# Kernel optimization log

Hardware: AMD Instinct MI355X
Metric: run time of the kernel (lower is better)

Reference implementation:

```python
import jax, jax.numpy as jnp
import numpy as np

NUM_CLASSES = 21
IOU_THRESH = 0.5
NEG_POS_RATIO = 3
VAR0, VAR1 = 0.1, 0.2


def point_form(priors):
    # (cx,cy,w,h) -> (xmin,ymin,xmax,ymax)
    return jnp.concatenate([priors[:, :2] - priors[:, 2:] / 2,
                            priors[:, :2] + priors[:, 2:] / 2], axis=-1)


def jaccard(box_a, box_b):
    # box_a: [n,4] point form, box_b: [N,4] point form -> [n,N]
    max_xy = jnp.minimum(box_a[:, None, 2:], box_b[None, :, 2:])
    min_xy = jnp.maximum(box_a[:, None, :2], box_b[None, :, :2])
    inter = jnp.prod(jnp.clip(max_xy - min_xy, 0.0, None), axis=-1)
    area_a = jnp.prod(box_a[:, 2:] - box_a[:, :2], axis=-1)[:, None]
    area_b = jnp.prod(box_b[:, 2:] - box_b[:, :2], axis=-1)[None, :]
    return inter / (area_a + area_b - inter)


def encode(matched, priors):
    # matched: [N,4] point form, priors: [N,4] center form
    g_cxcy = ((matched[:, :2] + matched[:, 2:]) / 2 - priors[:, :2]) / (VAR0 * priors[:, 2:])
    g_wh = jnp.log((matched[:, 2:] - matched[:, :2]) / priors[:, 2:]) / VAR1
    return jnp.concatenate([g_cxcy, g_wh], axis=-1)


def match_one(truths, labels, priors):
    # truths: [n_obj,4], labels: [n_obj], priors: [N,4] center form
    ov = jaccard(truths, point_form(priors))          # [n_obj, N]
    best_prior_idx = jnp.argmax(ov, axis=1)           # [n_obj]
    best_truth_overlap = jnp.max(ov, axis=0)          # [N]
    best_truth_idx = jnp.argmax(ov, axis=0)           # [N]
    best_truth_overlap = best_truth_overlap.at[best_prior_idx].set(2.0)
    def body(j, bti):
        return bti.at[best_prior_idx[j]].set(j)
    best_truth_idx = jax.lax.fori_loop(0, truths.shape[0], body, best_truth_idx)
    matched = truths[best_truth_idx]                  # [N,4]
    conf = labels[best_truth_idx].astype(jnp.int32) + 1
    conf = jnp.where(best_truth_overlap < IOU_THRESH, 0, conf)
    return encode(matched, priors), conf


def smooth_l1(x):
    ax = jnp.abs(x)
    return jnp.where(ax < 1.0, 0.5 * x * x, ax - 0.5)


def setup_inputs() -> dict:
    key = jax.random.key(0)
    k1, k2, k3, k4, k5, k6, k7 = jax.random.split(key, 7)
    B, N, n_obj = 128, 8732, 16
    loc_data = jax.random.normal(k1, (B, N, 4), jnp.float32)
    conf_data = jax.random.normal(k2, (B, N, NUM_CLASSES), jnp.float32)
    # valid ground-truth boxes in [0,1], point form, plus class label in [0,20)
    mins = jax.random.uniform(k3, (B, n_obj, 2)) * 0.6
    sizes = jax.random.uniform(k4, (B, n_obj, 2)) * 0.35 + 0.05
    labels = jax.random.randint(k5, (B, n_obj), 0, NUM_CLASSES - 1).astype(jnp.float32)
    targets = jnp.concatenate([mins, mins + sizes, labels[..., None]], axis=-1)
    # priors in center form with positive w,h
    centers = jax.random.uniform(k6, (N, 2))
    wh = jax.random.uniform(k7, (N, 2)) * 0.5 + 0.05
    priors = jnp.concatenate([centers, wh], axis=-1).astype(jnp.float32)
    return {"loc_data": loc_data, "conf_data": conf_data, "targets": targets, "priors": priors}


def _forward(loc_data, conf_data, targets, priors):
    B, N = loc_data.shape[0], loc_data.shape[1]
    truths, labels = targets[:, :, :4], targets[:, :, 4]
    target_loc, target_conf = jax.vmap(match_one, in_axes=(0, 0, None))(truths, labels, priors)
    pos = target_conf > 0                             # [B,N]
    # localization: smooth-L1 summed over positive priors
    loss_l = jnp.sum(smooth_l1(loc_data - target_loc) * pos[..., None].astype(loc_data.dtype))
    # per-prior CE surrogate: logsumexp - logit[target]
    lse = jax.nn.logsumexp(conf_data, axis=-1)        # [B,N]
    gathered = jnp.take_along_axis(conf_data, target_conf[..., None], axis=-1)[..., 0]
    loss_c_all = lse - gathered                       # [B,N]
    # hard negative mining via double argsort ranking (positives excluded)
    lc = jnp.where(pos, 0.0, loss_c_all)
    loss_idx = jnp.argsort(-lc, axis=1)
    idx_rank = jnp.argsort(loss_idx, axis=1)
    num_pos = jnp.sum(pos.astype(jnp.int32), axis=1, keepdims=True)   # [B,1]
    num_neg = jnp.minimum(NEG_POS_RATIO * num_pos, N - 1)
    neg = idx_rank < num_neg
    sel = pos | neg
    loss_c = jnp.sum(jnp.where(sel, loss_c_all, 0.0))
    n_total = jnp.sum(num_pos).astype(loc_data.dtype)
    return loss_l / n_total, loss_c / n_total


def reference(loc_data, conf_data, targets, priors):
    return _forward(loc_data, conf_data, targets, priors)
```

## Files before the change

kernel.cpp:

```cpp
#include <hip/hip_runtime.h>
#include <cstdint>
#include <cstddef>

#define HB1 4096
#define HB2 2048
#define CMAX 21
#define IOU_T 0.5f

__device__ __forceinline__ float sl1(float x) {
    float ax = fabsf(x);
    return ax < 1.0f ? 0.5f * x * x : ax - 0.5f;
}

__global__ __launch_bounds__(256) void kA_best_prior(
    const float* __restrict__ targets, const float* __restrict__ priors,
    float* __restrict__ bpi_val, int* __restrict__ bpi_idx,
    int* __restrict__ num_pos_g, float* __restrict__ accB_g,
    float* __restrict__ acc_g, unsigned* __restrict__ done_g,
    int N, int NOBJ, int SLICES, int CHUNK, int B)
{
    const int s = blockIdx.x, b = blockIdx.y, t = threadIdx.x;
    __shared__ float tb[16 * 4];
    __shared__ float ta[16];
    __shared__ float wv[4 * 16];
    __shared__ int   wi[4 * 16];

    if (s == 0 && b == 0) {
        for (int q = t; q < B; q += 256) num_pos_g[q] = 0;
        for (int q = t; q < 2 * B; q += 256) accB_g[q] = 0.f;
        if (t < 4) acc_g[t] = 0.f;
        if (t == 0) *done_g = 0u;
    }

    if (t < 16) {
        if (t < NOBJ) {
            const float* tr = targets + ((size_t)b * NOBJ + t) * 5;
            float x0 = tr[0], y0 = tr[1], x1 = tr[2], y1 = tr[3];
            tb[t * 4 + 0] = x0; tb[t * 4 + 1] = y0;
            tb[t * 4 + 2] = x1; tb[t * 4 + 3] = y1;
            ta[t] = (x1 - x0) * (y1 - y0);
        } else {
            tb[t * 4 + 0] = 0.f; tb[t * 4 + 1] = 0.f;
            tb[t * 4 + 2] = 0.f; tb[t * 4 + 3] = 0.f;
            ta[t] = 0.f;
        }
    }
    __syncthreads();

    float bv[16]; int bi[16];
#pragma unroll
    for (int j = 0; j < 16; j++) { bv[j] = -1.0f; bi[j] = 0x7fffffff; }

    const int start = s * CHUNK;
    const int end = min(start + CHUNK, N);
    for (int i = start + t; i < end; i += 256) {
        float4 p = ((const float4*)priors)[i];
        float bx0 = p.x - p.z * 0.5f, by0 = p.y - p.w * 0.5f;
        float bx1 = p.x + p.z * 0.5f, by1 = p.y + p.w * 0.5f;
        float ab = (bx1 - bx0) * (by1 - by0);
#pragma unroll
        for (int j = 0; j < 16; j++) {
            float iw = fminf(tb[j * 4 + 2], bx1) - fmaxf(tb[j * 4 + 0], bx0);
            float ih = fminf(tb[j * 4 + 3], by1) - fmaxf(tb[j * 4 + 1], by0);
            iw = fmaxf(iw, 0.f); ih = fmaxf(ih, 0.f);
            float inter = iw * ih;
            float iou = inter / (ta[j] + ab - inter);
            if (iou > bv[j] || (iou == bv[j] && i < bi[j])) { bv[j] = iou; bi[j] = i; }
        }
    }

#pragma unroll
    for (int off = 32; off >= 1; off >>= 1) {
#pragma unroll
        for (int j = 0; j < 16; j++) {
            float v2 = __shfl_down(bv[j], off, 64);
            int   i2 = __shfl_down(bi[j], off, 64);
            if (v2 > bv[j] || (v2 == bv[j] && i2 < bi[j])) { bv[j] = v2; bi[j] = i2; }
        }
    }
    const int wid = t >> 6, lane = t & 63;
    if (lane == 0) {
#pragma unroll
        for (int j = 0; j < 16; j++) { wv[wid * 16 + j] = bv[j]; wi[wid * 16 + j] = bi[j]; }
    }
    __syncthreads();
    if (t < 16) {
        float v = wv[t]; int idx = wi[t];
#pragma unroll
        for (int w = 1; w < 4; w++) {
            float v2 = wv[w * 16 + t]; int i2 = wi[w * 16 + t];
            if (v2 > v || (v2 == v && i2 < idx)) { v = v2; idx = i2; }
        }
        if (t < NOBJ) {
            int o = (b * SLICES + s) * 16 + t;
            bpi_val[o] = v;
            bpi_idx[o] = idx;
        }
    }
}

#define IOU_STEP(j) { \
    float4 tj = tb4[j]; \
    float taj = (tj.z - tj.x) * (tj.w - tj.y); \
    float iw = fminf(tj.z, bx1) - fmaxf(tj.x, bx0); \
    float ih = fminf(tj.w, by1) - fmaxf(tj.y, by0); \
    iw = fmaxf(iw, 0.f); ih = fmaxf(ih, 0.f); \
    float inter = iw * ih; \
    float iou = inter * __builtin_amdgcn_rcpf(taj + ab - inter); \
    if (iou > bto) { bto = iou; bti = (j); } }

__global__ __launch_bounds__(256, 3) void kB_main(
    const float* __restrict__ loc, const float* __restrict__ conf,
    const float* __restrict__ targets, const float* __restrict__ priors,
    const float* __restrict__ bpi_val, const int* __restrict__ bpi_idx,
    float* __restrict__ lc_out, int* __restrict__ num_pos, float* __restrict__ accB,
    int N, int NOBJ, int SLICES, int TPB, int BPB)
{
    const int g = blockIdx.x;
    const int b = g / BPB;
    const int j0 = g % BPB;
    const int t = threadIdx.x;
    const int wid = t >> 6, lane = t & 63;

    __shared__ __align__(16) float buf[2][256 * CMAX];
    __shared__ __align__(16) float tb[16 * 4];
    __shared__ float tl[16];
    __shared__ __align__(16) int bpi_s[16];
    __shared__ float wred[4 * 3];

    if (t < 16) {
        if (t < NOBJ) {
            const float* tr = targets + ((size_t)b * NOBJ + t) * 5;
            tb[t * 4 + 0] = tr[0]; tb[t * 4 + 1] = tr[1];
            tb[t * 4 + 2] = tr[2]; tb[t * 4 + 3] = tr[3];
            tl[t] = tr[4];
            float bv = -1.f; int bi = 0x7fffffff;
            for (int s2 = 0; s2 < SLICES; s2++) {
                int o = (b * SLICES + s2) * 16 + t;
                float v = bpi_val[o]; int idx = bpi_idx[o];
                if (v > bv || (v == bv && idx < bi)) { bv = v; bi = idx; }
            }
            bpi_s[t] = bi;
        } else {
            tb[t * 4 + 0] = 0.f; tb[t * 4 + 1] = 0.f; tb[t * 4 + 2] = 0.f; tb[t * 4 + 3] = 0.f;
            tl[t] = 0.f; bpi_s[t] = -1;
        }
    }

    const float* confB = conf + (size_t)b * N * CMAX;
    const float* locB  = loc + (size_t)b * N * 4;

    float4 r0, r1, r2, r3, r4, r5, pld, ppr;

    auto stage = [&](int xx) {
        int i0s = xx * 256;
        int rows_s = min(256, N - i0s);
        int nf4s = (rows_s * CMAX) >> 2;
        const float4* s4 = (const float4*)(confB + (size_t)i0s * CMAX);
        if (t + 0    < nf4s) r0 = s4[t + 0];
        if (t + 256  < nf4s) r1 = s4[t + 256];
        if (t + 512  < nf4s) r2 = s4[t + 512];
        if (t + 768  < nf4s) r3 = s4[t + 768];
        if (t + 1024 < nf4s) r4 = s4[t + 1024];
        if (t + 1280 < nf4s) r5 = s4[t + 1280];
        if (t < rows_s) {
            ppr = ((const float4*)priors)[i0s + t];
            pld = ((const float4*)locB)[i0s + t];
        }
    };

    float ll = 0.f, plc = 0.f, np = 0.f;
    int x = j0, p = 0;
    if (x < TPB) stage(x);

    while (x < TPB) {
        const int i0 = x * 256;
        const int rows = min(256, N - i0);
        const int nf4 = (rows * CMAX) >> 2;

        float4 myp = ppr, myl = pld;

        float4* bp4f = (float4*)buf[p];
        if (t + 0    < nf4) bp4f[t + 0]    = r0;
        if (t + 256  < nf4) bp4f[t + 256]  = r1;
        if (t + 512  < nf4) bp4f[t + 512]  = r2;
        if (t + 768  < nf4) bp4f[t + 768]  = r3;
        if (t + 1024 < nf4) bp4f[t + 1024] = r4;
        if (t + 1280 < nf4) bp4f[t + 1280] = r5;
        __syncthreads();

        int xn = x + BPB;
        if (xn < TPB) stage(xn);

        if (t < rows) {
            const int i = i0 + t;
            float4 pp = myp;
            float bx0 = pp.x - pp.z * 0.5f, by0 = pp.y - pp.w * 0.5f;
            float bx1 = pp.x + pp.z * 0.5f, by1 = pp.y + pp.w * 0.5f;
            float ab = (bx1 - bx0) * (by1 - by0);
            float bto = -1.f; int bti = 0;
            const float4* tb4 = (const float4*)tb;
            if (NOBJ == 16) {
#pragma unroll
                for (int j = 0; j < 16; j++) IOU_STEP(j);
            } else {
                for (int j = 0; j < NOBJ; j++) IOU_STEP(j);
            }
            const int4* bp4 = (const int4*)bpi_s;
#pragma unroll
            for (int jj = 0; jj < 4; jj++) {
                int4 q = bp4[jj];
                if (q.x == i) { bto = 2.0f; bti = jj * 4 + 0; }
                if (q.y == i) { bto = 2.0f; bti = jj * 4 + 1; }
                if (q.z == i) { bto = 2.0f; bti = jj * 4 + 2; }
                if (q.w == i) { bto = 2.0f; bti = jj * 4 + 3; }
            }
            bool pos = !(bto < IOU_T);
            if (pos) {
                float4 tj = tb4[bti];
                float rz = __builtin_amdgcn_rcpf(pp.z);
                float rw = __builtin_amdgcn_rcpf(pp.w);
                float gcx = ((tj.x + tj.z) * 0.5f - pp.x) * (10.0f * rz);
                float gcy = ((tj.y + tj.w) * 0.5f - pp.y) * (10.0f * rw);
                float gw = __logf((tj.z - tj.x) * rz) * 5.0f;
                float gh = __logf((tj.w - tj.y) * rw) * 5.0f;
                ll += sl1(myl.x - gcx) + sl1(myl.y - gcy) + sl1(myl.z - gw) + sl1(myl.w - gh);
                np += 1.f;
            }
            int cf = pos ? ((int)tl[bti] + 1) : 0;
            const float* cr = buf[p] + t * CMAX;
            float m = cr[0];
#pragma unroll
            for (int c = 1; c < CMAX; c++) m = fmaxf(m, cr[c]);
            float ssum = 0.f;
#pragma unroll
            for (int c = 0; c < CMAX; c++) ssum += __expf(cr[c] - m);
            float lse = m + __logf(ssum);
            float lossc = lse - cr[cf];
            if (pos) plc += lossc;
            float lcv = pos ? 0.f : lossc;
            lcv = fmaxf(lcv, 0.f);
            lc_out[(size_t)b * N + i] = lcv;
        }
        p ^= 1;
        x = xn;
    }

#pragma unroll
    for (int off = 32; off >= 1; off >>= 1) {
        ll  += __shfl_down(ll, off, 64);
        plc += __shfl_down(plc, off, 64);
        np  += __shfl_down(np, off, 64);
    }
    if (lane == 0) { wred[wid * 3 + 0] = ll; wred[wid * 3 + 1] = plc; wred[wid * 3 + 2] = np; }
    __syncthreads();
    if (t == 0) {
        float a0 = 0.f, a1 = 0.f, a2 = 0.f;
#pragma unroll
        for (int w = 0; w < 4; w++) { a0 += wred[w * 3 + 0]; a1 += wred[w * 3 + 1]; a2 += wred[w * 3 + 2]; }
        atomicAdd(&accB[b * 2 + 0], a0);
        atomicAdd(&accB[b * 2 + 1], a1);
        atomicAdd(&num_pos[b], (int)a2);
    }
}

__device__ __forceinline__ void suffix_scan(int* cnt, float* sm, int n, int t, int nt) {
    for (int d = 1; d < n; d <<= 1) {
        int tc[8]; float ts[8];
        int r = 0;
        for (int q = t; q < n; q += nt, r++) {
            int src = q + d;
            tc[r] = (src < n) ? cnt[src] : 0;
            ts[r] = (src < n) ? sm[src] : 0.f;
        }
        __syncthreads();
        r = 0;
        for (int q = t; q < n; q += nt, r++) { cnt[q] += tc[r]; sm[q] += ts[r]; }
        __syncthreads();
    }
}

__global__ __launch_bounds__(512) void kC_topk(
    const float* __restrict__ lc, const int* __restrict__ num_pos,
    const float* __restrict__ accB,
    float* __restrict__ acc, unsigned* __restrict__ done_ctr,
    float* __restrict__ out, int N, int B)
{
    const int b = blockIdx.x, t = threadIdx.x;
    const int NT = 512;
    __shared__ int cnt[HB1];
    __shared__ float sm[HB1];
    __shared__ int s_strad, s_krem;
    __shared__ float s_above;
    __shared__ int s_last;
    __shared__ float wsum[8], wsA[8], wsB[8];

    const int k = min(3 * num_pos[b], N - 1);
    const float* lcb = lc + (size_t)b * N;
    float total = 0.f;

    if (k > 0) {
        for (int q = t; q < HB1; q += NT) { cnt[q] = 0; sm[q] = 0.f; }
        __syncthreads();
        const int n4 = N >> 2;
        const float4* lcb4 = (const float4*)lcb;
        for (int i = t; i < n4; i += NT) {
            float4 v = lcb4[i];
            { unsigned u = __float_as_uint(v.x) >> 19; atomicAdd(&cnt[u], 1); atomicAdd(&sm[u], v.x); }
            { unsigned u = __float_as_uint(v.y) >> 19; atomicAdd(&cnt[u], 1); atomicAdd(&sm[u], v.y); }
            { unsigned u = __float_as_uint(v.z) >> 19; atomicAdd(&cnt[u], 1); atomicAdd(&sm[u], v.z); }
            { unsigned u = __float_as_uint(v.w) >> 19; atomicAdd(&cnt[u], 1); atomicAdd(&sm[u], v.w); }
        }
        for (int i = (n4 << 2) + t; i < N; i += NT) {
            float v = lcb[i];
            unsigned u = __float_as_uint(v) >> 19;
            atomicAdd(&cnt[u], 1); atomicAdd(&sm[u], v);
        }
        __syncthreads();
        suffix_scan(cnt, sm, HB1, t, NT);
        for (int q = t; q < HB1; q += NT) {
            int incl = cnt[q];
            int excl = (q < HB1 - 1) ? cnt[q + 1] : 0;
            if (excl < k && k <= incl) {
                s_strad = q; s_krem = k - excl;
                s_above = (q < HB1 - 1) ? sm[q + 1] : 0.f;
            }
        }
        __syncthreads();
        int s1 = s_strad, k2 = s_krem;
        total += s_above;
        __syncthreads();

        for (int q = t; q < HB2; q += NT) { cnt[q] = 0; sm[q] = 0.f; }
        __syncthreads();
        for (int i = t; i < N; i += NT) {
            float v = lcb[i];
            unsigned u = __float_as_uint(v);
            if ((int)(u >> 19) == s1) {
                int q = (int)((u >> 8) & 0x7FF);
                atomicAdd(&cnt[q], 1); atomicAdd(&sm[q], v);
            }
        }
        __syncthreads();
        suffix_scan(cnt, sm, HB2, t, NT);
        for (int q = t; q < HB2; q += NT) {
            int incl = cnt[q];
            int excl = (q < HB2 - 1) ? cnt[q + 1] : 0;
            if (excl < k2 && k2 <= incl) {
                s_strad = q; s_krem = k2 - excl;
                s_above = (q < HB2 - 1) ? sm[q + 1] : 0.f;
            }
        }
        __syncthreads();
        int s2 = s_strad, krem = s_krem;
        total += s_above;
        float tval = __uint_as_float((((unsigned)s1) << 19) | (((unsigned)s2) << 8));
        total += (float)krem * tval;
    }

    if (t == 0) {
        if (k > 0) atomicAdd(&acc[1], total);
        __threadfence();
        unsigned old = atomicAdd(done_ctr, 1u);
        s_last = (old == (unsigned)gridDim.x - 1u) ? 1 : 0;
    }
    __syncthreads();
    if (s_last) {
        __threadfence();
        float vn = 0.f, va = 0.f, vb = 0.f;
        for (int q = t; q < B; q += NT) {
            vn += (float)num_pos[q];
            va += accB[q * 2 + 0];
            vb += accB[q * 2 + 1];
        }
#pragma unroll
        for (int off = 32; off >= 1; off >>= 1) {
            vn += __shfl_down(vn, off, 64);
            va += __shfl_down(va, off, 64);
            vb += __shfl_down(vb, off, 64);
        }
        if ((t & 63) == 0) { wsum[t >> 6] = vn; wsA[t >> 6] = va; wsB[t >> 6] = vb; }
        __syncthreads();
        if (t == 0) {
            float n = 0.f, a = 0.f, bsum = 0.f;
#pragma unroll
            for (int w = 0; w < 8; w++) { n += wsum[w]; a += wsA[w]; bsum += wsB[w]; }
            float l2 = atomicAdd(&acc[1], 0.0f);
            out[0] = a / n;
            out[1] = (bsum + l2) / n;
        }
    }
}

extern "C" void kernel_launch(void* const* d_in, const int* in_sizes, int n_in,
                              void* d_out, int out_size, void* d_ws, size_t ws_size,
                              hipStream_t stream)
{
    const float* loc     = (const float*)d_in[0];
    const float* conf    = (const float*)d_in[1];
    const float* targets = (const float*)d_in[2];
    const float* priors  = (const float*)d_in[3];
    float* out = (float*)d_out;

    const int N = in_sizes[3] / 4;
    const int BN = in_sizes[0] / 4;
    const int B = BN / N;
    const int NOBJ = in_sizes[2] / (B * 5);
    const int SLICES = 8;
    const int CHUNK = (N + SLICES - 1) / SLICES;
    const int TPB = (N + 255) / 256;
    const int BPB = 6;

    char* w = (char*)d_ws;
    float*    lc_ws   = (float*)w;                         size_t off = (size_t)BN * 4;
    float*    bpi_val = (float*)(w + off);                 off += (size_t)B * SLICES * 16 * 4;
    int*      bpi_idx = (int*)(w + off);                   off += (size_t)B * SLICES * 16 * 4;
    int*      num_pos = (int*)(w + off);                   off += (size_t)B * 4;
    float*    accB    = (float*)(w + off);                 off += (size_t)B * 2 * 4;
    float*    acc     = (float*)(w + off);                 off += 16;
    unsigned* done    = (unsigned*)(w + off);              off += 16;

    dim3 gA(SLICES, B);
    kA_best_prior<<<gA, 256, 0, stream>>>(targets, priors, bpi_val, bpi_idx,
                                          num_pos, accB, acc, done, N, NOBJ, SLICES, CHUNK, B);

    kB_main<<<B * BPB, 256, 0, stream>>>(loc, conf, targets, priors, bpi_val, bpi_idx,
                                         lc_ws, num_pos, accB, N, NOBJ, SLICES, TPB, BPB);

    kC_topk<<<B, 512, 0, stream>>>(lc_ws, num_pos, accB, acc, done, out, N, B);
}
```

Measured before the change: 261.2 us.

## Replace shared-memory Hillis-Steele suffix scan with wave-shuffle scan in top-k kernel

The histogram-based top-k kernel replaces its log-step shared-memory suffix scan over 4096/2048 bins with a per-thread vector load, a 64-lane shuffle suffix scan and a cross-wave combine. The block size doubles to 1024 threads so each thread owns exactly 4 or 2 bins. This removes the many barrier-separated passes over shared memory. The trade-off is a larger block, which may lower occupancy and raise contention on the shared-memory histogram atomics.

```diff
diff --git a/kernel.cpp b/kernel.cpp
--- a/kernel.cpp
+++ b/kernel.cpp
@@ -264,43 +264,40 @@
     }
 }
 
-__device__ __forceinline__ void suffix_scan(int* cnt, float* sm, int n, int t, int nt) {
-    for (int d = 1; d < n; d <<= 1) {
-        int tc[8]; float ts[8];
-        int r = 0;
-        for (int q = t; q < n; q += nt, r++) {
-            int src = q + d;
-            tc[r] = (src < n) ? cnt[src] : 0;
-            ts[r] = (src < n) ? sm[src] : 0.f;
-        }
-        __syncthreads();
-        r = 0;
-        for (int q = t; q < n; q += nt, r++) { cnt[q] += tc[r]; sm[q] += ts[r]; }
-        __syncthreads();
-    }
-}
-
-__global__ __launch_bounds__(512) void kC_topk(
+__device__ __forceinline__ void wave_sufscan(int& c, float& s, int lane) {
+#pragma unroll
+    for (int off = 1; off < 64; off <<= 1) {
+        int c2 = __shfl_down(c, off, 64);
+        float s2 = __shfl_down(s, off, 64);
+        if (lane + off < 64) { c += c2; s += s2; }
+    }
+}
+
+__global__ __launch_bounds__(1024) void kC_topk(
     const float* __restrict__ lc, const int* __restrict__ num_pos,
     const float* __restrict__ accB,
     float* __restrict__ acc, unsigned* __restrict__ done_ctr,
     float* __restrict__ out, int N, int B)
 {
     const int b = blockIdx.x, t = threadIdx.x;
-    const int NT = 512;
-    __shared__ int cnt[HB1];
-    __shared__ float sm[HB1];
+    const int NT = 1024;
+    const int wid = t >> 6, lane = t & 63;
+    __shared__ __align__(16) int   cnt[HB1];
+    __shared__ __align__(16) float sm[HB1];
+    __shared__ int   wc[16];
+    __shared__ float ws[16];
     __shared__ int s_strad, s_krem;
     __shared__ float s_above;
     __shared__ int s_last;
-    __shared__ float wsum[8], wsA[8], wsB[8];
+    __shared__ float wsum[16], wsA[16], wsB[16];
 
     const int k = min(3 * num_pos[b], N - 1);
     const float* lcb = lc + (size_t)b * N;
     float total = 0.f;
 
     if (k > 0) {
-        for (int q = t; q < HB1; q += NT) { cnt[q] = 0; sm[q] = 0.f; }
+        ((int4*)cnt)[t] = make_int4(0, 0, 0, 0);
+        ((float4*)sm)[t] = make_float4(0.f, 0.f, 0.f, 0.f);
         __syncthreads();
         const int n4 = N >> 2;
         const float4* lcb4 = (const float4*)lcb;
@@ -317,21 +314,33 @@
             atomicAdd(&cnt[u], 1); atomicAdd(&sm[u], v);
         }
         __syncthreads();
-        suffix_scan(cnt, sm, HB1, t, NT);
-        for (int q = t; q < HB1; q += NT) {
-            int incl = cnt[q];
-            int excl = (q < HB1 - 1) ? cnt[q + 1] : 0;
-            if (excl < k && k <= incl) {
-                s_strad = q; s_krem = k - excl;
-                s_above = (q < HB1 - 1) ? sm[q + 1] : 0.f;
-            }
-        }
-        __syncthreads();
-        int s1 = s_strad, k2 = s_krem;
+        {
+            int4  cv = ((const int4*)cnt)[t];
+            float4 sv = ((const float4*)sm)[t];
+            int   ci = cv.x + cv.y + cv.z + cv.w;
+            float si = sv.x + sv.y + sv.z + sv.w;
+            wave_sufscan(ci, si, lane);
+            if (lane == 0) { wc[wid] = ci; ws[wid] = si; }
+            __syncthreads();
+            int cab = 0; float sab = 0.f;
+            for (int w = wid + 1; w < 16; w++) { cab += wc[w]; sab += ws[w]; }
+            int   i0c = ci + cab;          float f0 = si + sab;
+            int   i1c = i0c - cv.x;        float f1 = f0 - sv.x;
+            int   i2c = i1c - cv.y;        float f2 = f1 - sv.y;
+            int   i3c = i2c - cv.z;        float f3 = f2 - sv.z;
+            int   i4c = i3c - cv.w;
+            if (i1c < k && k <= i0c) { s_strad = 4 * t + 0; s_krem = k - i1c; s_above = f1; }
+            if (i2c < k && k <= i1c) { s_strad = 4 * t + 1; s_krem = k - i2c; s_above = f2; }
+            if (i3c < k && k <= i2c) { s_strad = 4 * t + 2; s_krem = k - i3c; s_above = f3; }
+            if (i4c < k && k <= i3c) { s_strad = 4 * t + 3; s_krem = k - i4c; s_above = f3 - sv.w; }
+        }
+        __syncthreads();
+        const int s1 = s_strad, k2 = s_krem;
         total += s_above;
-        __syncthreads();
-
-        for (int q = t; q < HB2; q += NT) { cnt[q] = 0; sm[q] = 0.f; }
+
+        __syncthreads();
+        ((int2*)cnt)[t] = make_int2(0, 0);
+        ((float2*)sm)[t] = make_float2(0.f, 0.f);
         __syncthreads();
         for (int i = t; i < N; i += NT) {
             float v = lcb[i];
@@ -342,17 +351,24 @@
             }
         }
         __syncthreads();
-        suffix_scan(cnt, sm, HB2, t, NT);
-        for (int q = t; q < HB2; q += NT) {
-            int incl = cnt[q];
-            int excl = (q < HB2 - 1) ? cnt[q + 1] : 0;
-            if (excl < k2 && k2 <= incl) {
-                s_strad = q; s_krem = k2 - excl;
-                s_above = (q < HB2 - 1) ? sm[q + 1] : 0.f;
-            }
-        }
-        __syncthreads();
-        int s2 = s_strad, krem = s_krem;
+        {
+            int2  cv = ((const int2*)cnt)[t];
+            float2 sv = ((const float2*)sm)[t];
+            int   ci = cv.x + cv.y;
+            float si = sv.x + sv.y;
+            wave_sufscan(ci, si, lane);
+            if (lane == 0) { wc[wid] = ci; ws[wid] = si; }
+            __syncthreads();
+            int cab = 0; float sab = 0.f;
+            for (int w = wid + 1; w < 16; w++) { cab += wc[w]; sab += ws[w]; }
+            int   i0c = ci + cab;       float f0 = si + sab;
+            int   i1c = i0c - cv.x;     float f1 = f0 - sv.x;
+            int   i2c = i1c - cv.y;
+            if (i1c < k2 && k2 <= i0c) { s_strad = 2 * t + 0; s_krem = k2 - i1c; s_above = f1; }
+            if (i2c < k2 && k2 <= i1c) { s_strad = 2 * t + 1; s_krem = k2 - i2c; s_above = f1 - sv.y; }
+        }
+        __syncthreads();
+        const int s2 = s_strad, krem = s_krem;
         total += s_above;
         float tval = __uint_as_float((((unsigned)s1) << 19) | (((unsigned)s2) << 8));
         total += (float)krem * tval;
@@ -379,12 +395,12 @@
             va += __shfl_down(va, off, 64);
             vb += __shfl_down(vb, off, 64);
         }
-        if ((t & 63) == 0) { wsum[t >> 6] = vn; wsA[t >> 6] = va; wsB[t >> 6] = vb; }
+        if (lane == 0) { wsum[wid] = vn; wsA[wid] = va; wsB[wid] = vb; }
         __syncthreads();
         if (t == 0) {
             float n = 0.f, a = 0.f, bsum = 0.f;
 #pragma unroll
-            for (int w = 0; w < 8; w++) { n += wsum[w]; a += wsA[w]; bsum += wsB[w]; }
+            for (int w = 0; w < 16; w++) { n += wsum[w]; a += wsA[w]; bsum += wsB[w]; }
             float l2 = atomicAdd(&acc[1], 0.0f);
             out[0] = a / n;
             out[1] = (bsum + l2) / n;
@@ -427,5 +443,5 @@
     kB_main<<<B * BPB, 256, 0, stream>>>(loc, conf, targets, priors, bpi_val, bpi_idx,
                                          lc_ws, num_pos, accB, N, NOBJ, SLICES, TPB, BPB);
 
-    kC_topk<<<B, 512, 0, stream>>>(lc_ws, num_pos, accB, acc, done, out, N, B);
-}
+    kC_topk<<<B, 1024, 0, stream>>>(lc_ws, num_pos, accB, acc, done, out, N, B);
+}
```

Result: faster. 225.7 us (median of 2 runs) (-13.6%).
